# Kernel tuning notes

Measured on AMD Instinct MI355X. Metric: run time of the kernel, lower is better.

## Reference

```python
import jax, jax.numpy as jnp
import numpy as np

M, B, U, D = 65536, 128, 256, 512
USAGE_DECAY = 0.95

def _l2n(x, axis):
    # tf.nn.l2_normalize semantics (K.l2_normalize)
    return x / jnp.sqrt(jnp.maximum(jnp.sum(x * x, axis=axis, keepdims=True), 1e-12))

def _lstm_cell(x, h, c, kernel, rec_kernel, bias):
    # Keras LSTMCell: gates in order i, f, c, o
    z = x @ kernel + h @ rec_kernel + bias  # [B, 4U]
    zi, zf, zc, zo = jnp.split(z, 4, axis=-1)
    i = jax.nn.sigmoid(zi)
    f = jax.nn.sigmoid(zf)
    c_new = f * c + i * jnp.tanh(zc)
    o = jax.nn.sigmoid(zo)
    h_new = o * jnp.tanh(c_new)
    return h_new, c_new

def setup_inputs() -> dict:
    key = jax.random.key(0)
    ks = jax.random.split(key, 10)
    return {
        "inputs": jax.random.normal(ks[0], (B, D), jnp.float32),
        "r_tm1": jnp.zeros((B, U), jnp.float32),
        "m_tm1": jax.random.uniform(ks[1], (M, U), jnp.float32),
        "c_wu_tm1": jax.random.uniform(ks[2], (M, B), jnp.float32),
        "c_wlu_tm1": jnp.zeros((M, B), jnp.float32),
        "c_wr_tm1": jax.random.uniform(ks[3], (M, B), jnp.float32),
        "h_tm1": jax.random.normal(ks[4], (B, U), jnp.float32) * 0.1,
        "cc_tm1": jax.random.normal(ks[5], (B, U), jnp.float32) * 0.1,
        "kernel": jax.random.normal(ks[6], (D + U, 4 * U), jnp.float32) * 0.02,
        "rec_kernel": jax.random.normal(ks[7], (U, 4 * U), jnp.float32) * 0.02,
        "bias": jnp.zeros((4 * U,), jnp.float32),
        "write_gate": jax.random.normal(ks[8], (1,), jnp.float32),
    }

def reference(inputs, r_tm1, m_tm1, c_wu_tm1, c_wlu_tm1, c_wr_tm1,
              h_tm1, cc_tm1, kernel, rec_kernel, bias, write_gate):
    # Controller step on [inputs, r_tm1]
    ctrl_in = jnp.concatenate([inputs, r_tm1], axis=1)          # [B, D+U]
    key_list, cc = _lstm_cell(ctrl_in, h_tm1, cc_tm1, kernel, rec_kernel, bias)  # [B, U]

    wg = jax.nn.sigmoid(write_gate)                              # [1]
    # NOTE: faithful to source -- scalar (1 - wg) is ADDED elementwise, then c_wlu added
    c_ww = wg * c_wr_tm1 + (1.0 - wg) + c_wlu_tm1                # [M, B]

    # cosine-similarity addressing
    cos = _l2n(key_list, 1) @ _l2n(m_tm1, 1).T                   # [B, M]
    # K.softmax on the transposed matrix => softmax over the BATCH axis (faithful)
    c_wr = jax.nn.softmax(cos.T, axis=-1)                        # [M, B]
    read = c_wr.T @ m_tm1                                        # [B, U]

    c_wu = USAGE_DECAY * c_wu_tm1 + c_wr + c_ww                  # [M, B]

    # top_k(c_wu.T, M): v.T[-1,:] is the per-batch minimum over slots
    mins = jnp.min(c_wu, axis=0)                                 # [B]
    min_idx = jnp.argmin(c_wu, axis=0)                           # [B]
    b_star = jnp.argmin(mins)                                    # scalar
    i_star = min_idx[b_star]                                     # global least-used slot

    c_wlu = (c_wu <= mins[None, :]).astype(jnp.float32)          # [M, B]

    # zeroing_matrix = one_hot(i_star broadcast to B cols, on=0, off=1) [M,B];
    # dot(zeroing[M,B], ones[B,U]) -> rows = B except zeroed row (faithful B scaling)
    keep = 1.0 - jax.nn.one_hot(i_star, M, dtype=jnp.float32)    # [M]
    memory = (float(B) * keep)[:, None] * m_tm1                  # [M, U]
    memory = c_ww @ key_list + memory                            # [M, U]

    return (read, memory, c_wu, c_wlu, c_wr, key_list, cc)
```

## Files before the change

### kernel.cpp

```cpp
#include <hip/hip_runtime.h>
#include <math.h>

#define NM 65536
#define NB 128
#define NU 256
#define ND 512

constexpr size_t OUT_READ = 0;
constexpr size_t OUT_MEM  = 32768;
constexpr size_t OUT_CWU  = OUT_MEM + 16777216;
constexpr size_t OUT_CWLU = OUT_CWU + 8388608;
constexpr size_t OUT_CWR  = OUT_CWLU + 8388608;
constexpr size_t OUT_KEY  = OUT_CWR + 8388608;
constexpr size_t OUT_CC   = OUT_KEY + 32768;

constexpr size_t WS_KLNT   = 0;
constexpr size_t WS_MINENC = 131072;
constexpr size_t WS_MINS   = 132096;
constexpr size_t WS_ISTAR  = 132608;
constexpr size_t WS_PART   = 135168;

__device__ __forceinline__ unsigned fenc(float x) {
    unsigned u = __float_as_uint(x);
    return (u & 0x80000000u) ? ~u : (u | 0x80000000u);
}
__device__ __forceinline__ float fdec(unsigned e) {
    unsigned u = (e & 0x80000000u) ? (e ^ 0x80000000u) : ~e;
    return __uint_as_float(u);
}
__device__ __forceinline__ float sigm(float x) { return 1.0f / (1.0f + expf(-x)); }

__global__ __launch_bounds__(256) void k_lstm(
    const float* __restrict__ xin_g, const float* __restrict__ r_tm1,
    const float* __restrict__ h_tm1, const float* __restrict__ cc_tm1,
    const float* __restrict__ Wk, const float* __restrict__ Wr,
    const float* __restrict__ bias, float* __restrict__ out,
    float* __restrict__ klnT, unsigned long long* __restrict__ minenc)
{
    const int b = blockIdx.x, t = threadIdx.x;
    __shared__ float xin[ND + NU];
    __shared__ float hh[NU];
    __shared__ float red[NU];
    for (int k = t; k < ND; k += 256) xin[k] = xin_g[b * ND + k];
    xin[ND + t] = r_tm1[b * NU + t];
    hh[t] = h_tm1[b * NU + t];
    out[OUT_READ + b * NU + t] = 0.f;
    if (b == 0 && t < NB) minenc[t] = ~0ULL;
    __syncthreads();

    float zi = bias[t], zf = bias[NU + t], zc = bias[2 * NU + t], zo = bias[3 * NU + t];
    #pragma unroll 4
    for (int k = 0; k < ND + NU; ++k) {
        const float x = xin[k];
        const float* w = Wk + (size_t)k * (4 * NU);
        zi += x * w[t]; zf += x * w[NU + t]; zc += x * w[2 * NU + t]; zo += x * w[3 * NU + t];
    }
    #pragma unroll 4
    for (int k = 0; k < NU; ++k) {
        const float x = hh[k];
        const float* w = Wr + (size_t)k * (4 * NU);
        zi += x * w[t]; zf += x * w[NU + t]; zc += x * w[2 * NU + t]; zo += x * w[3 * NU + t];
    }
    const float gi = sigm(zi), gf = sigm(zf), gc = tanhf(zc), go = sigm(zo);
    const float cold = cc_tm1[b * NU + t];
    const float cn = __fadd_rn(__fmul_rn(gf, cold), __fmul_rn(gi, gc));
    const float hn = __fmul_rn(go, tanhf(cn));
    out[OUT_KEY + b * NU + t] = hn;
    out[OUT_CC + b * NU + t] = cn;
    red[t] = hn * hn;
    __syncthreads();
    for (int s = 128; s > 0; s >>= 1) { if (t < s) red[t] += red[t + s]; __syncthreads(); }
    const float nrm = sqrtf(fmaxf(red[0], 1e-12f));
    klnT[t * NB + b] = hn / nrm;
}

__global__ __launch_bounds__(256, 2) void k_dot(
    const float* __restrict__ mT, const float* __restrict__ klnT,
    const float* __restrict__ cwr_t, const float* __restrict__ cwlu_t,
    const float* __restrict__ cwu_t, const float* __restrict__ wgp,
    float* __restrict__ out, unsigned long long* __restrict__ minenc)
{
    __shared__ float smem[16384];
    __shared__ float rn_s[128];
    const int t = threadIdx.x, w = t >> 6, l = t & 63;
    const int tx = t & 15, ty = t >> 4;
    const int b0 = tx * 8, s0 = ty * 8;
    const int sb = blockIdx.x * 128;

    #pragma unroll 4
    for (int i = 0; i < 32; ++i) {
        const int s = w * 32 + i;
        const float4 mv = *(const float4*)(mT + (size_t)(sb + s) * NU + l * 4);
        float ss = mv.x * mv.x + mv.y * mv.y + mv.z * mv.z + mv.w * mv.w;
        #pragma unroll
        for (int d = 1; d < 64; d <<= 1) ss += __shfl_xor(ss, d);
        if (l == 0) rn_s[s] = sqrtf(fmaxf(ss, 1e-12f));
    }

    const int sl = t & 127, ug = t >> 7;
    const int ku_ = t >> 4, kb = (t & 15) * 4;

    float acc[8][8];
    #pragma unroll
    for (int i = 0; i < 8; ++i)
        #pragma unroll
        for (int j = 0; j < 8; ++j) acc[i][j] = 0.f;

    float4 gm[2], gk[2];
    #pragma unroll
    for (int i = 0; i < 2; ++i) {
        gm[i] = *(const float4*)(mT + (size_t)(sb + sl) * NU + (ug + 2 * i) * 4);
        gk[i] = *(const float4*)(klnT + (size_t)ku_ * NB + kb + i * 64);
    }
    for (int c = 0; c < 16; ++c) {
        const int mo = (c & 1) * 2048;
        const int ko = 4096 + (c & 1) * 2048;
        #pragma unroll
        for (int i = 0; i < 2; ++i) {
            const int uo = (ug + 2 * i) * 4;
            smem[mo + (uo + 0) * 128 + sl] = gm[i].x;
            smem[mo + (uo + 1) * 128 + sl] = gm[i].y;
            smem[mo + (uo + 2) * 128 + sl] = gm[i].z;
            smem[mo + (uo + 3) * 128 + sl] = gm[i].w;
            *(float4*)&smem[ko + ku_ * 128 + kb + i * 64] = gk[i];
        }
        __syncthreads();
        if (c < 15) {
            const int uc = (c + 1) * 16;
            #pragma unroll
            for (int i = 0; i < 2; ++i) {
                gm[i] = *(const float4*)(mT + (size_t)(sb + sl) * NU + uc + (ug + 2 * i) * 4);
                gk[i] = *(const float4*)(klnT + (size_t)(uc + ku_) * NB + kb + i * 64);
            }
        }
        #pragma unroll 4
        for (int u = 0; u < 16; ++u) {
            const float4 sv0 = *(const float4*)&smem[mo + u * 128 + s0];
            const float4 sv1 = *(const float4*)&smem[mo + u * 128 + s0 + 4];
            const float4 kv0 = *(const float4*)&smem[ko + u * 128 + b0];
            const float4 kv1 = *(const float4*)&smem[ko + u * 128 + b0 + 4];
            const float sv[8] = {sv0.x, sv0.y, sv0.z, sv0.w, sv1.x, sv1.y, sv1.z, sv1.w};
            const float kv[8] = {kv0.x, kv0.y, kv0.z, kv0.w, kv1.x, kv1.y, kv1.z, kv1.w};
            #pragma unroll
            for (int i = 0; i < 8; ++i)
                #pragma unroll
                for (int j = 0; j < 8; ++j)
                    acc[i][j] += sv[i] * kv[j];
        }
        __syncthreads();
    }

    #pragma unroll
    for (int i = 0; i < 8; ++i) {
        *(float4*)&smem[(s0 + i) * 128 + b0]     = make_float4(acc[i][0], acc[i][1], acc[i][2], acc[i][3]);
        *(float4*)&smem[(s0 + i) * 128 + b0 + 4] = make_float4(acc[i][4], acc[i][5], acc[i][6], acc[i][7]);
    }
    __syncthreads();

    const float wg = sigm(wgp[0]);
    const float omw = __fsub_rn(1.f, wg);
    unsigned long long lmin0 = ~0ULL, lmin1 = ~0ULL;
    #pragma unroll 2
    for (int i = 0; i < 32; ++i) {
        const int s = w * 32 + i;
        const int m = sb + s;
        const float2 dv = *(const float2*)&smem[s * 128 + 2 * l];
        const float rnv = rn_s[s];
        const float2 wrt = ((const float2*)(cwr_t + (size_t)m * NB))[l];
        const float2 wlu = ((const float2*)(cwlu_t + (size_t)m * NB))[l];
        const float2 wut = ((const float2*)(cwu_t + (size_t)m * NB))[l];
        const float c0 = dv.x / rnv, c1 = dv.y / rnv;
        float mx = fmaxf(c0, c1);
        #pragma unroll
        for (int d = 1; d < 64; d <<= 1) mx = fmaxf(mx, __shfl_xor(mx, d));
        const float e0 = expf(c0 - mx), e1 = expf(c1 - mx);
        float sm = e0 + e1;
        #pragma unroll
        for (int d = 1; d < 64; d <<= 1) sm += __shfl_xor(sm, d);
        const float w0 = e0 / sm, w1 = e1 / sm;
        const float cww0 = __fadd_rn(__fadd_rn(__fmul_rn(wg, wrt.x), omw), wlu.x);
        const float cww1 = __fadd_rn(__fadd_rn(__fmul_rn(wg, wrt.y), omw), wlu.y);
        const float cu0 = __fadd_rn(__fadd_rn(__fmul_rn(0.95f, wut.x), w0), cww0);
        const float cu1 = __fadd_rn(__fadd_rn(__fmul_rn(0.95f, wut.y), w1), cww1);
        ((float2*)(out + OUT_CWR))[(size_t)m * 64 + l] = make_float2(w0, w1);
        ((float2*)(out + OUT_CWU))[(size_t)m * 64 + l] = make_float2(cu0, cu1);
        const unsigned long long e0u = (((unsigned long long)fenc(cu0)) << 32) | (unsigned)m;
        const unsigned long long e1u = (((unsigned long long)fenc(cu1)) << 32) | (unsigned)m;
        lmin0 = (e0u < lmin0) ? e0u : lmin0;
        lmin1 = (e1u < lmin1) ? e1u : lmin1;
    }
    atomicMin(&minenc[2 * l], lmin0);
    atomicMin(&minenc[2 * l + 1], lmin1);
}

__global__ void k_argmin(const unsigned long long* __restrict__ minenc,
                         float* __restrict__ mins, unsigned* __restrict__ istar)
{
    __shared__ unsigned long long red[NB];
    const int t = threadIdx.x;
    const unsigned long long e = minenc[t];
    const unsigned enc32 = (unsigned)(e >> 32);
    mins[t] = fdec(enc32);
    red[t] = (((unsigned long long)enc32) << 32) | (unsigned)t;
    __syncthreads();
    for (int s = 64; s > 0; s >>= 1) {
        if (t < s) { const unsigned long long o = red[t + s]; if (o < red[t]) red[t] = o; }
        __syncthreads();
    }
    if (t == 0) {
        const unsigned bstar = (unsigned)(red[0] & 0xFFFFFFFFu);
        istar[0] = (unsigned)(minenc[bstar] & 0xFFFFFFFFu);
    }
}

__global__ __launch_bounds__(256, 1) void k_mem(
    const float* __restrict__ mT,
    const float* __restrict__ cwr_t, const float* __restrict__ cwlu_t,
    const float* __restrict__ wgp, const float* __restrict__ mins,
    const unsigned* __restrict__ istar_p, float* __restrict__ out)
{
    __shared__ float key[NB][NU];
    __shared__ float cww[32][NB];
    __shared__ float minsb[NB];
    const int t = threadIdx.x, w = t >> 6, l = t & 63;
    const int u0 = l * 4;
    const int sl = t >> 3, sb = (t & 7) * 16;

    for (int i = t; i < NB * NU / 4; i += 256)
        ((float4*)key)[i] = ((const float4*)(out + OUT_KEY))[i];
    if (t < NB) minsb[t] = mins[t];

    const float wg = sigm(wgp[0]);
    const float omw = __fsub_rn(1.f, wg);
    const int istar = (int)istar_p[0];
    const int base = blockIdx.x * 256;

    float4 wr[4], lu[4], wu[4], pm[8];
    #pragma unroll
    for (int k = 0; k < 4; ++k) {
        const size_t row = (size_t)(base + sl) * NB + sb + 4 * k;
        wr[k] = *(const float4*)(cwr_t + row);
        lu[k] = *(const float4*)(cwlu_t + row);
        wu[k] = *(const float4*)(out + OUT_CWU + row);
    }
    #pragma unroll
    for (int j = 0; j < 8; ++j)
        pm[j] = *(const float4*)(mT + (size_t)(base + w * 8 + j) * NU + u0);
    __syncthreads();

    for (int p = 0; p < 8; ++p) {
        const int sp = base + p * 32;
        #pragma unroll
        for (int k = 0; k < 4; ++k) {
            float4 cw;
            cw.x = __fadd_rn(__fadd_rn(__fmul_rn(wg, wr[k].x), omw), lu[k].x);
            cw.y = __fadd_rn(__fadd_rn(__fmul_rn(wg, wr[k].y), omw), lu[k].y);
            cw.z = __fadd_rn(__fadd_rn(__fmul_rn(wg, wr[k].z), omw), lu[k].z);
            cw.w = __fadd_rn(__fadd_rn(__fmul_rn(wg, wr[k].w), omw), lu[k].w);
            *(float4*)&cww[sl][sb + 4 * k] = cw;
            const float4 mb = *(const float4*)&minsb[sb + 4 * k];
            float4 wl;
            wl.x = (wu[k].x <= mb.x) ? 1.f : 0.f;
            wl.y = (wu[k].y <= mb.y) ? 1.f : 0.f;
            wl.z = (wu[k].z <= mb.z) ? 1.f : 0.f;
            wl.w = (wu[k].w <= mb.w) ? 1.f : 0.f;
            *(float4*)(out + OUT_CWLU + (size_t)(sp + sl) * NB + sb + 4 * k) = wl;
        }
        __syncthreads();
        float4 pmn[8];
        if (p < 7) {
            #pragma unroll
            for (int k = 0; k < 4; ++k) {
                const size_t row = (size_t)(sp + 32 + sl) * NB + sb + 4 * k;
                wr[k] = *(const float4*)(cwr_t + row);
                lu[k] = *(const float4*)(cwlu_t + row);
                wu[k] = *(const float4*)(out + OUT_CWU + row);
            }
            #pragma unroll
            for (int j = 0; j < 8; ++j)
                pmn[j] = *(const float4*)(mT + (size_t)(sp + 32 + w * 8 + j) * NU + u0);
        }
        float4 acc[8];
        #pragma unroll
        for (int j = 0; j < 8; ++j) acc[j] = make_float4(0.f, 0.f, 0.f, 0.f);
        for (int b0 = 0; b0 < NB; b0 += 4) {
            const float4 kv0 = *(const float4*)&key[b0 + 0][u0];
            const float4 kv1 = *(const float4*)&key[b0 + 1][u0];
            const float4 kv2 = *(const float4*)&key[b0 + 2][u0];
            const float4 kv3 = *(const float4*)&key[b0 + 3][u0];
            #pragma unroll
            for (int j = 0; j < 8; ++j) {
                const float4 cw = *(const float4*)&cww[w * 8 + j][b0];
                acc[j].x += cw.x * kv0.x; acc[j].y += cw.x * kv0.y; acc[j].z += cw.x * kv0.z; acc[j].w += cw.x * kv0.w;
                acc[j].x += cw.y * kv1.x; acc[j].y += cw.y * kv1.y; acc[j].z += cw.y * kv1.z; acc[j].w += cw.y * kv1.w;
                acc[j].x += cw.z * kv2.x; acc[j].y += cw.z * kv2.y; acc[j].z += cw.z * kv2.z; acc[j].w += cw.z * kv2.w;
                acc[j].x += cw.w * kv3.x; acc[j].y += cw.w * kv3.y; acc[j].z += cw.w * kv3.z; acc[j].w += cw.w * kv3.w;
            }
        }
        #pragma unroll
        for (int j = 0; j < 8; ++j) {
            const int s = sp + w * 8 + j;
            const float kf = (s == istar) ? 0.f : 128.f;
            float4 o;
            o.x = acc[j].x + kf * pm[j].x;
            o.y = acc[j].y + kf * pm[j].y;
            o.z = acc[j].z + kf * pm[j].z;
            o.w = acc[j].w + kf * pm[j].w;
            *(float4*)(out + OUT_MEM + (size_t)s * NU + u0) = o;
            if (p < 7) pm[j] = pmn[j];
        }
        __syncthreads();
    }
}

template <int USE_PART>
__global__ __launch_bounds__(256) void k_read(
    const float* __restrict__ mT, float* __restrict__ out, float* __restrict__ part)
{
    __shared__ float m_ch[2][8][128];
    __shared__ float cwr_ch[2][8][128];
    const int t = threadIdx.x;
    const int r = blockIdx.x, ri = r >> 1, uh = r & 1;
    const int s0 = ri * 256;
    const int b0 = (t & 15) * 8, u0 = (t >> 4) * 8;
    const int ssl = t >> 5, sul = (t & 31) * 4;

    float4 acc[8][2];
    #pragma unroll
    for (int bi = 0; bi < 8; ++bi) { acc[bi][0] = make_float4(0,0,0,0); acc[bi][1] = make_float4(0,0,0,0); }

    float4 pm = *(const float4*)(mT + (size_t)(s0 + ssl) * NU + uh * 128 + sul);
    float4 pc = *(const float4*)(out + OUT_CWR + (size_t)(s0 + ssl) * NB + sul);

    for (int c = 0; c < 32; ++c) {
        const int buf = c & 1;
        *(float4*)&m_ch[buf][ssl][sul] = pm;
        *(float4*)&cwr_ch[buf][ssl][sul] = pc;
        __syncthreads();
        if (c + 1 < 32) {
            const size_t sn = (size_t)(s0 + (c + 1) * 8 + ssl);
            pm = *(const float4*)(mT + sn * NU + uh * 128 + sul);
            pc = *(const float4*)(out + OUT_CWR + sn * NB + sul);
        }
        #pragma unroll
        for (int sj = 0; sj < 8; ++sj) {
            const float4 ca = *(const float4*)&cwr_ch[buf][sj][b0];
            const float4 cb = *(const float4*)&cwr_ch[buf][sj][b0 + 4];
            const float4 ma = *(const float4*)&m_ch[buf][sj][u0];
            const float4 mb = *(const float4*)&m_ch[buf][sj][u0 + 4];
            const float cwa[8] = {ca.x, ca.y, ca.z, ca.w, cb.x, cb.y, cb.z, cb.w};
            #pragma unroll
            for (int bi = 0; bi < 8; ++bi) {
                acc[bi][0].x += cwa[bi] * ma.x; acc[bi][0].y += cwa[bi] * ma.y;
                acc[bi][0].z += cwa[bi] * ma.z; acc[bi][0].w += cwa[bi] * ma.w;
                acc[bi][1].x += cwa[bi] * mb.x; acc[bi][1].y += cwa[bi] * mb.y;
                acc[bi][1].z += cwa[bi] * mb.z; acc[bi][1].w += cwa[bi] * mb.w;
            }
        }
    }

    if (USE_PART) {
        float* dst = part + (size_t)r * (128 * 128);
        #pragma unroll
        for (int bi = 0; bi < 8; ++bi) {
            *(float4*)(dst + (size_t)(b0 + bi) * 128 + u0) = acc[bi][0];
            *(float4*)(dst + (size_t)(b0 + bi) * 128 + u0 + 4) = acc[bi][1];
        }
    } else {
        #pragma unroll
        for (int bi = 0; bi < 8; ++bi) {
            const float v[8] = {acc[bi][0].x, acc[bi][0].y, acc[bi][0].z, acc[bi][0].w,
                                acc[bi][1].x, acc[bi][1].y, acc[bi][1].z, acc[bi][1].w};
            #pragma unroll
            for (int q = 0; q < 8; ++q)
                atomicAdd(out + OUT_READ + (size_t)(b0 + bi) * NU + uh * 128 + u0 + q, v[q]);
        }
    }
}

__global__ __launch_bounds__(256) void k_redread(const float* __restrict__ part,
                                                 float* __restrict__ out)
{
    const int b = blockIdx.x, u = threadIdx.x;
    const int uh = u >> 7, ul = u & 127;
    float s = 0.f;
    #pragma unroll 4
    for (int ri = 0; ri < 256; ++ri)
        s += part[((size_t)(ri * 2 + uh) * 128 + b) * 128 + ul];
    out[OUT_READ + b * NU + u] = s;
}

extern "C" void kernel_launch(void* const* d_in, const int* in_sizes, int n_in,
                              void* d_out, int out_size, void* d_ws, size_t ws_size,
                              hipStream_t stream)
{
    const float* inputs    = (const float*)d_in[0];
    const float* r_tm1     = (const float*)d_in[1];
    const float* m_tm1     = (const float*)d_in[2];
    const float* c_wu_tm1  = (const float*)d_in[3];
    const float* c_wlu_tm1 = (const float*)d_in[4];
    const float* c_wr_tm1  = (const float*)d_in[5];
    const float* h_tm1     = (const float*)d_in[6];
    const float* cc_tm1    = (const float*)d_in[7];
    const float* Wk        = (const float*)d_in[8];
    const float* Wr        = (const float*)d_in[9];
    const float* bias      = (const float*)d_in[10];
    const float* wgate     = (const float*)d_in[11];
    float* out = (float*)d_out;
    char* ws = (char*)d_ws;

    float* klnT = (float*)(ws + WS_KLNT);
    unsigned long long* minenc = (unsigned long long*)(ws + WS_MINENC);
    float* mins = (float*)(ws + WS_MINS);
    unsigned* istar = (unsigned*)(ws + WS_ISTAR);
    float* part = (float*)(ws + WS_PART);
    const bool use_part = ws_size >= WS_PART + (size_t)512 * 128 * 128 * 4;

    hipLaunchKernelGGL(k_lstm, dim3(128), dim3(256), 0, stream,
                       inputs, r_tm1, h_tm1, cc_tm1, Wk, Wr, bias, out, klnT, minenc);
    hipLaunchKernelGGL(k_dot, dim3(512), dim3(256), 0, stream,
                       m_tm1, klnT, c_wr_tm1, c_wlu_tm1, c_wu_tm1, wgate, out, minenc);
    hipLaunchKernelGGL(k_argmin, dim3(1), dim3(128), 0, stream, minenc, mins, istar);
    hipLaunchKernelGGL(k_mem, dim3(256), dim3(256), 0, stream,
                       m_tm1, c_wr_tm1, c_wlu_tm1, wgate, mins, istar, out);
    if (use_part) {
        hipLaunchKernelGGL((k_read<1>), dim3(512), dim3(256), 0, stream, m_tm1, out, part);
        hipLaunchKernelGGL(k_redread, dim3(128), dim3(256), 0, stream, part, out);
    } else {
        hipLaunchKernelGGL((k_read<0>), dim3(512), dim3(256), 0, stream, m_tm1, out, part);
    }
}
```

Baseline: 467.1 us.

## Shrink k_dot shared memory by streaming key tiles from registers and chunked epilogue

Restructures the cosine-similarity GEMM in k_dot. The key matrix is no longer staged in LDS; each thread keeps a small rotating register ring of key rows loaded straight from global/L2. Only 8-row memory slices are double-buffered in shared memory, and a single barrier per chunk replaces the previous two. The epilogue drains the accumulator tile in four 32-row chunks through a small padded buffer. Together these cut LDS from about 64KB to about 25KB, so more blocks can be resident per CU. The cost is more barriers in the epilogue, redundant global loads of the key matrix, and a changed thread-to-output mapping (strided rows and columns) that must stay consistent.

```diff
diff --git a/kernel.cpp b/kernel.cpp
--- a/kernel.cpp
+++ b/kernel.cpp
@@ -80,12 +80,13 @@
     const float* __restrict__ cwu_t, const float* __restrict__ wgp,
     float* __restrict__ out, unsigned long long* __restrict__ minenc)
 {
-    __shared__ float smem[16384];
+    __shared__ float ms[2][8][128];
+    __shared__ float sp[32][132];
     __shared__ float rn_s[128];
     const int t = threadIdx.x, w = t >> 6, l = t & 63;
     const int tx = t & 15, ty = t >> 4;
-    const int b0 = tx * 8, s0 = ty * 8;
     const int sb = blockIdx.x * 128;
+    const int sl = t & 127, ug = t >> 7;
 
     #pragma unroll 4
     for (int i = 0; i < 32; ++i) {
@@ -97,97 +98,95 @@
         if (l == 0) rn_s[s] = sqrtf(fmaxf(ss, 1e-12f));
     }
 
-    const int sl = t & 127, ug = t >> 7;
-    const int ku_ = t >> 4, kb = (t & 15) * 4;
-
     float acc[8][8];
     #pragma unroll
     for (int i = 0; i < 8; ++i)
         #pragma unroll
         for (int j = 0; j < 8; ++j) acc[i][j] = 0.f;
 
-    float4 gm[2], gk[2];
-    #pragma unroll
-    for (int i = 0; i < 2; ++i) {
-        gm[i] = *(const float4*)(mT + (size_t)(sb + sl) * NU + (ug + 2 * i) * 4);
-        gk[i] = *(const float4*)(klnT + (size_t)ku_ * NB + kb + i * 64);
-    }
-    for (int c = 0; c < 16; ++c) {
-        const int mo = (c & 1) * 2048;
-        const int ko = 4096 + (c & 1) * 2048;
-        #pragma unroll
-        for (int i = 0; i < 2; ++i) {
-            const int uo = (ug + 2 * i) * 4;
-            smem[mo + (uo + 0) * 128 + sl] = gm[i].x;
-            smem[mo + (uo + 1) * 128 + sl] = gm[i].y;
-            smem[mo + (uo + 2) * 128 + sl] = gm[i].z;
-            smem[mo + (uo + 3) * 128 + sl] = gm[i].w;
-            *(float4*)&smem[ko + ku_ * 128 + kb + i * 64] = gk[i];
-        }
-        __syncthreads();
-        if (c < 15) {
-            const int uc = (c + 1) * 16;
-            #pragma unroll
-            for (int i = 0; i < 2; ++i) {
-                gm[i] = *(const float4*)(mT + (size_t)(sb + sl) * NU + uc + (ug + 2 * i) * 4);
-                gk[i] = *(const float4*)(klnT + (size_t)(uc + ku_) * NB + kb + i * 64);
-            }
-        }
-        #pragma unroll 4
-        for (int u = 0; u < 16; ++u) {
-            const float4 sv0 = *(const float4*)&smem[mo + u * 128 + s0];
-            const float4 sv1 = *(const float4*)&smem[mo + u * 128 + s0 + 4];
-            const float4 kv0 = *(const float4*)&smem[ko + u * 128 + b0];
-            const float4 kv1 = *(const float4*)&smem[ko + u * 128 + b0 + 4];
-            const float sv[8] = {sv0.x, sv0.y, sv0.z, sv0.w, sv1.x, sv1.y, sv1.z, sv1.w};
-            const float kv[8] = {kv0.x, kv0.y, kv0.z, kv0.w, kv1.x, kv1.y, kv1.z, kv1.w};
+    float4 kva[4], kvb[4];
+    #pragma unroll
+    for (int u = 0; u < 4; ++u) {
+        kva[u] = *(const float4*)(klnT + (size_t)u * NB + tx * 4);
+        kvb[u] = *(const float4*)(klnT + (size_t)u * NB + tx * 4 + 64);
+    }
+    float4 gm = *(const float4*)(mT + (size_t)(sb + sl) * NU + ug * 4);
+
+    for (int c = 0; c < 32; ++c) {
+        const int cb = c & 1;
+        ms[cb][ug * 4 + 0][sl] = gm.x;
+        ms[cb][ug * 4 + 1][sl] = gm.y;
+        ms[cb][ug * 4 + 2][sl] = gm.z;
+        ms[cb][ug * 4 + 3][sl] = gm.w;
+        if (c < 31)
+            gm = *(const float4*)(mT + (size_t)(sb + sl) * NU + (c + 1) * 8 + ug * 4);
+        __syncthreads();
+        #pragma unroll
+        for (int u8 = 0; u8 < 8; ++u8) {
+            const int r = u8 & 3;
+            const float4 sv0 = *(const float4*)&ms[cb][u8][ty * 4];
+            const float4 sv1 = *(const float4*)&ms[cb][u8][64 + ty * 4];
+            const float svv[8] = {sv0.x, sv0.y, sv0.z, sv0.w, sv1.x, sv1.y, sv1.z, sv1.w};
+            const float kvv[8] = {kva[r].x, kva[r].y, kva[r].z, kva[r].w,
+                                  kvb[r].x, kvb[r].y, kvb[r].z, kvb[r].w};
             #pragma unroll
             for (int i = 0; i < 8; ++i)
                 #pragma unroll
                 for (int j = 0; j < 8; ++j)
-                    acc[i][j] += sv[i] * kv[j];
-        }
-        __syncthreads();
-    }
-
-    #pragma unroll
-    for (int i = 0; i < 8; ++i) {
-        *(float4*)&smem[(s0 + i) * 128 + b0]     = make_float4(acc[i][0], acc[i][1], acc[i][2], acc[i][3]);
-        *(float4*)&smem[(s0 + i) * 128 + b0 + 4] = make_float4(acc[i][4], acc[i][5], acc[i][6], acc[i][7]);
-    }
-    __syncthreads();
+                    acc[i][j] += svv[i] * kvv[j];
+            const int un = (c * 8 + u8 + 4) & 255;
+            kva[r] = *(const float4*)(klnT + (size_t)un * NB + tx * 4);
+            kvb[r] = *(const float4*)(klnT + (size_t)un * NB + tx * 4 + 64);
+        }
+    }
 
     const float wg = sigm(wgp[0]);
     const float omw = __fsub_rn(1.f, wg);
     unsigned long long lmin0 = ~0ULL, lmin1 = ~0ULL;
-    #pragma unroll 2
-    for (int i = 0; i < 32; ++i) {
-        const int s = w * 32 + i;
-        const int m = sb + s;
-        const float2 dv = *(const float2*)&smem[s * 128 + 2 * l];
-        const float rnv = rn_s[s];
-        const float2 wrt = ((const float2*)(cwr_t + (size_t)m * NB))[l];
-        const float2 wlu = ((const float2*)(cwlu_t + (size_t)m * NB))[l];
-        const float2 wut = ((const float2*)(cwu_t + (size_t)m * NB))[l];
-        const float c0 = dv.x / rnv, c1 = dv.y / rnv;
-        float mx = fmaxf(c0, c1);
-        #pragma unroll
-        for (int d = 1; d < 64; d <<= 1) mx = fmaxf(mx, __shfl_xor(mx, d));
-        const float e0 = expf(c0 - mx), e1 = expf(c1 - mx);
-        float sm = e0 + e1;
-        #pragma unroll
-        for (int d = 1; d < 64; d <<= 1) sm += __shfl_xor(sm, d);
-        const float w0 = e0 / sm, w1 = e1 / sm;
-        const float cww0 = __fadd_rn(__fadd_rn(__fmul_rn(wg, wrt.x), omw), wlu.x);
-        const float cww1 = __fadd_rn(__fadd_rn(__fmul_rn(wg, wrt.y), omw), wlu.y);
-        const float cu0 = __fadd_rn(__fadd_rn(__fmul_rn(0.95f, wut.x), w0), cww0);
-        const float cu1 = __fadd_rn(__fadd_rn(__fmul_rn(0.95f, wut.y), w1), cww1);
-        ((float2*)(out + OUT_CWR))[(size_t)m * 64 + l] = make_float2(w0, w1);
-        ((float2*)(out + OUT_CWU))[(size_t)m * 64 + l] = make_float2(cu0, cu1);
-        const unsigned long long e0u = (((unsigned long long)fenc(cu0)) << 32) | (unsigned)m;
-        const unsigned long long e1u = (((unsigned long long)fenc(cu1)) << 32) | (unsigned)m;
-        lmin0 = (e0u < lmin0) ? e0u : lmin0;
-        lmin1 = (e1u < lmin1) ? e1u : lmin1;
+    #pragma unroll
+    for (int g = 0; g < 4; ++g) {
+        if ((ty >> 3) == (g & 1)) {
+            const int h = g >> 1;
+            const int sl0 = (ty & 7) * 4;
+            #pragma unroll
+            for (int q = 0; q < 4; ++q) {
+                *(float4*)&sp[sl0 + q][tx * 4] =
+                    make_float4(acc[h * 4 + q][0], acc[h * 4 + q][1], acc[h * 4 + q][2], acc[h * 4 + q][3]);
+                *(float4*)&sp[sl0 + q][64 + tx * 4] =
+                    make_float4(acc[h * 4 + q][4], acc[h * 4 + q][5], acc[h * 4 + q][6], acc[h * 4 + q][7]);
+            }
+        }
+        __syncthreads();
+        #pragma unroll 2
+        for (int i = 0; i < 8; ++i) {
+            const int s = 32 * g + w * 8 + i;
+            const int m = sb + s;
+            const float2 dv = *(const float2*)&sp[s - 32 * g][2 * l];
+            const float rnv = rn_s[s];
+            const float2 wrt = ((const float2*)(cwr_t + (size_t)m * NB))[l];
+            const float2 wlu = ((const float2*)(cwlu_t + (size_t)m * NB))[l];
+            const float2 wut = ((const float2*)(cwu_t + (size_t)m * NB))[l];
+            const float c0 = dv.x / rnv, c1 = dv.y / rnv;
+            float mx = fmaxf(c0, c1);
+            #pragma unroll
+            for (int d = 1; d < 64; d <<= 1) mx = fmaxf(mx, __shfl_xor(mx, d));
+            const float e0 = expf(c0 - mx), e1 = expf(c1 - mx);
+            float sm = e0 + e1;
+            #pragma unroll
+            for (int d = 1; d < 64; d <<= 1) sm += __shfl_xor(sm, d);
+            const float w0 = e0 / sm, w1 = e1 / sm;
+            const float cww0 = __fadd_rn(__fadd_rn(__fmul_rn(wg, wrt.x), omw), wlu.x);
+            const float cww1 = __fadd_rn(__fadd_rn(__fmul_rn(wg, wrt.y), omw), wlu.y);
+            const float cu0 = __fadd_rn(__fadd_rn(__fmul_rn(0.95f, wut.x), w0), cww0);
+            const float cu1 = __fadd_rn(__fadd_rn(__fmul_rn(0.95f, wut.y), w1), cww1);
+            ((float2*)(out + OUT_CWR))[(size_t)m * 64 + l] = make_float2(w0, w1);
+            ((float2*)(out + OUT_CWU))[(size_t)m * 64 + l] = make_float2(cu0, cu1);
+            const unsigned long long e0u = (((unsigned long long)fenc(cu0)) << 32) | (unsigned)m;
+            const unsigned long long e1u = (((unsigned long long)fenc(cu1)) << 32) | (unsigned)m;
+            lmin0 = (e0u < lmin0) ? e0u : lmin0;
+            lmin1 = (e1u < lmin1) ? e1u : lmin1;
+        }
+        __syncthreads();
     }
     atomicMin(&minenc[2 * l], lmin0);
     atomicMin(&minenc[2 * l + 1], lmin1);
```

Result: no change. 472.6 us (+1.2%).

## Compute memory update GEMM with bf16 MFMA instead of fp32 FMA loops

Applied to the files above, without the earlier changes.

The k_mem kernel's c_ww @ key_list product is rewritten to use bf16 MFMA 16x16x32 instructions. c_ww and a transposed key tile are converted to bf16 in shared memory, and the grid is doubled to 512 blocks of 128 slots with two blocks per CU. This targets the scalar fp32 FMA cost of the M×B×U GEMM. It reduces precision of the memory output to bf16 inputs and drops the software prefetch of m_tm1, whose scalar non-vectorized loads and stores in the epilogue may cost bandwidth.

```diff
diff --git a/kernel.cpp b/kernel.cpp
--- a/kernel.cpp
+++ b/kernel.cpp
@@ -1,4 +1,5 @@
 #include <hip/hip_runtime.h>
+#include <hip/hip_bf16.h>
 #include <math.h>
 
 #define NM 65536
@@ -20,6 +21,9 @@
 constexpr size_t WS_ISTAR  = 132608;
 constexpr size_t WS_PART   = 135168;
 
+typedef __attribute__((ext_vector_type(8))) short short8v;
+typedef __attribute__((ext_vector_type(4))) float floatx4;
+
 __device__ __forceinline__ unsigned fenc(float x) {
     unsigned u = __float_as_uint(x);
     return (u & 0x80000000u) ? ~u : (u | 0x80000000u);
@@ -29,6 +33,10 @@
     return __uint_as_float(u);
 }
 __device__ __forceinline__ float sigm(float x) { return 1.0f / (1.0f + expf(-x)); }
+__device__ __forceinline__ unsigned short f2b(float f) {
+    __hip_bfloat16 h = __float2bfloat16(f);
+    return *reinterpret_cast<unsigned short*>(&h);
+}
 
 __global__ __launch_bounds__(256) void k_lstm(
     const float* __restrict__ xin_g, const float* __restrict__ r_tm1,
@@ -213,103 +221,99 @@
     }
 }
 
-__global__ __launch_bounds__(256, 1) void k_mem(
+__global__ __launch_bounds__(256, 2) void k_mem(
     const float* __restrict__ mT,
     const float* __restrict__ cwr_t, const float* __restrict__ cwlu_t,
     const float* __restrict__ wgp, const float* __restrict__ mins,
     const unsigned* __restrict__ istar_p, float* __restrict__ out)
 {
-    __shared__ float key[NB][NU];
-    __shared__ float cww[32][NB];
-    __shared__ float minsb[NB];
+    __shared__ unsigned short cwwb[128 * 136];
+    __shared__ unsigned short keyT[128 * 136];
     const int t = threadIdx.x, w = t >> 6, l = t & 63;
-    const int u0 = l * 4;
-    const int sl = t >> 3, sb = (t & 7) * 16;
-
-    for (int i = t; i < NB * NU / 4; i += 256)
-        ((float4*)key)[i] = ((const float4*)(out + OUT_KEY))[i];
-    if (t < NB) minsb[t] = mins[t];
-
+    const int sb = blockIdx.x * 128;
     const float wg = sigm(wgp[0]);
     const float omw = __fsub_rn(1.f, wg);
     const int istar = (int)istar_p[0];
-    const int base = blockIdx.x * 256;
-
-    float4 wr[4], lu[4], wu[4], pm[8];
-    #pragma unroll
-    for (int k = 0; k < 4; ++k) {
-        const size_t row = (size_t)(base + sl) * NB + sb + 4 * k;
-        wr[k] = *(const float4*)(cwr_t + row);
-        lu[k] = *(const float4*)(cwlu_t + row);
-        wu[k] = *(const float4*)(out + OUT_CWU + row);
-    }
-    #pragma unroll
-    for (int j = 0; j < 8; ++j)
-        pm[j] = *(const float4*)(mT + (size_t)(base + w * 8 + j) * NU + u0);
-    __syncthreads();
-
-    for (int p = 0; p < 8; ++p) {
-        const int sp = base + p * 32;
-        #pragma unroll
-        for (int k = 0; k < 4; ++k) {
+
+    {
+        const int srow = t >> 5;
+        const int bc = (t & 31) * 4;
+        for (int it = 0; it < 16; ++it) {
+            const int s = it * 8 + srow;
+            const size_t row = (size_t)(sb + s) * NB + bc;
+            const float4 wr = *(const float4*)(cwr_t + row);
+            const float4 lu = *(const float4*)(cwlu_t + row);
+            const float4 wu = *(const float4*)(out + OUT_CWU + row);
             float4 cw;
-            cw.x = __fadd_rn(__fadd_rn(__fmul_rn(wg, wr[k].x), omw), lu[k].x);
-            cw.y = __fadd_rn(__fadd_rn(__fmul_rn(wg, wr[k].y), omw), lu[k].y);
-            cw.z = __fadd_rn(__fadd_rn(__fmul_rn(wg, wr[k].z), omw), lu[k].z);
-            cw.w = __fadd_rn(__fadd_rn(__fmul_rn(wg, wr[k].w), omw), lu[k].w);
-            *(float4*)&cww[sl][sb + 4 * k] = cw;
-            const float4 mb = *(const float4*)&minsb[sb + 4 * k];
+            cw.x = __fadd_rn(__fadd_rn(__fmul_rn(wg, wr.x), omw), lu.x);
+            cw.y = __fadd_rn(__fadd_rn(__fmul_rn(wg, wr.y), omw), lu.y);
+            cw.z = __fadd_rn(__fadd_rn(__fmul_rn(wg, wr.z), omw), lu.z);
+            cw.w = __fadd_rn(__fadd_rn(__fmul_rn(wg, wr.w), omw), lu.w);
+            ushort4 pk;
+            pk.x = f2b(cw.x); pk.y = f2b(cw.y); pk.z = f2b(cw.z); pk.w = f2b(cw.w);
+            *(ushort4*)&cwwb[s * 136 + bc] = pk;
+            const float4 mb = *(const float4*)(mins + bc);
             float4 wl;
-            wl.x = (wu[k].x <= mb.x) ? 1.f : 0.f;
-            wl.y = (wu[k].y <= mb.y) ? 1.f : 0.f;
-            wl.z = (wu[k].z <= mb.z) ? 1.f : 0.f;
-            wl.w = (wu[k].w <= mb.w) ? 1.f : 0.f;
-            *(float4*)(out + OUT_CWLU + (size_t)(sp + sl) * NB + sb + 4 * k) = wl;
+            wl.x = (wu.x <= mb.x) ? 1.f : 0.f;
+            wl.y = (wu.y <= mb.y) ? 1.f : 0.f;
+            wl.z = (wu.z <= mb.z) ? 1.f : 0.f;
+            wl.w = (wu.w <= mb.w) ? 1.f : 0.f;
+            *(float4*)(out + OUT_CWLU + row) = wl;
+        }
+    }
+
+    const int rk = (l >> 4) * 8;
+    const int rr = l & 15;
+
+    for (int uh = 0; uh < 2; ++uh) {
+        if (uh) __syncthreads();
+        {
+            const int br = t >> 5;
+            const int ko = (t & 31) * 4;
+            for (int it = 0; it < 16; ++it) {
+                const int b = it * 8 + br;
+                const float4 kv = *(const float4*)(out + OUT_KEY + (size_t)b * NU + uh * 128 + ko);
+                keyT[(ko + 0) * 136 + b] = f2b(kv.x);
+                keyT[(ko + 1) * 136 + b] = f2b(kv.y);
+                keyT[(ko + 2) * 136 + b] = f2b(kv.z);
+                keyT[(ko + 3) * 136 + b] = f2b(kv.w);
+            }
         }
         __syncthreads();
-        float4 pmn[8];
-        if (p < 7) {
-            #pragma unroll
-            for (int k = 0; k < 4; ++k) {
-                const size_t row = (size_t)(sp + 32 + sl) * NB + sb + 4 * k;
-                wr[k] = *(const float4*)(cwr_t + row);
-                lu[k] = *(const float4*)(cwlu_t + row);
-                wu[k] = *(const float4*)(out + OUT_CWU + row);
+
+        floatx4 acc0[8], acc1[8];
+        #pragma unroll
+        for (int ut = 0; ut < 8; ++ut) {
+            acc0[ut] = (floatx4){0.f, 0.f, 0.f, 0.f};
+            acc1[ut] = (floatx4){0.f, 0.f, 0.f, 0.f};
+        }
+        #pragma unroll
+        for (int kc = 0; kc < 4; ++kc) {
+            const short8v a0 = *(const short8v*)&cwwb[(w * 32 + rr) * 136 + kc * 32 + rk];
+            const short8v a1 = *(const short8v*)&cwwb[(w * 32 + 16 + rr) * 136 + kc * 32 + rk];
+            #pragma unroll
+            for (int ut = 0; ut < 8; ++ut) {
+                const short8v bf = *(const short8v*)&keyT[(ut * 16 + rr) * 136 + kc * 32 + rk];
+                acc0[ut] = __builtin_amdgcn_mfma_f32_16x16x32_bf16(a0, bf, acc0[ut], 0, 0, 0);
+                acc1[ut] = __builtin_amdgcn_mfma_f32_16x16x32_bf16(a1, bf, acc1[ut], 0, 0, 0);
             }
-            #pragma unroll
-            for (int j = 0; j < 8; ++j)
-                pmn[j] = *(const float4*)(mT + (size_t)(sp + 32 + w * 8 + j) * NU + u0);
-        }
-        float4 acc[8];
-        #pragma unroll
-        for (int j = 0; j < 8; ++j) acc[j] = make_float4(0.f, 0.f, 0.f, 0.f);
-        for (int b0 = 0; b0 < NB; b0 += 4) {
-            const float4 kv0 = *(const float4*)&key[b0 + 0][u0];
-            const float4 kv1 = *(const float4*)&key[b0 + 1][u0];
-            const float4 kv2 = *(const float4*)&key[b0 + 2][u0];
-            const float4 kv3 = *(const float4*)&key[b0 + 3][u0];
-            #pragma unroll
-            for (int j = 0; j < 8; ++j) {
-                const float4 cw = *(const float4*)&cww[w * 8 + j][b0];
-                acc[j].x += cw.x * kv0.x; acc[j].y += cw.x * kv0.y; acc[j].z += cw.x * kv0.z; acc[j].w += cw.x * kv0.w;
-                acc[j].x += cw.y * kv1.x; acc[j].y += cw.y * kv1.y; acc[j].z += cw.y * kv1.z; acc[j].w += cw.y * kv1.w;
-                acc[j].x += cw.z * kv2.x; acc[j].y += cw.z * kv2.y; acc[j].z += cw.z * kv2.z; acc[j].w += cw.z * kv2.w;
-                acc[j].x += cw.w * kv3.x; acc[j].y += cw.w * kv3.y; acc[j].z += cw.w * kv3.z; acc[j].w += cw.w * kv3.w;
+        }
+
+        #pragma unroll
+        for (int ut = 0; ut < 8; ++ut) {
+            const int gcol = uh * 128 + ut * 16 + rr;
+            #pragma unroll
+            for (int q = 0; q < 4; ++q) {
+                const int grow0 = sb + w * 32 + (l >> 4) * 4 + q;
+                const int grow1 = grow0 + 16;
+                const float mv0 = mT[(size_t)grow0 * NU + gcol];
+                const float mv1 = mT[(size_t)grow1 * NU + gcol];
+                const float kf0 = (grow0 == istar) ? 0.f : 128.f;
+                const float kf1 = (grow1 == istar) ? 0.f : 128.f;
+                out[OUT_MEM + (size_t)grow0 * NU + gcol] = acc0[ut][q] + kf0 * mv0;
+                out[OUT_MEM + (size_t)grow1 * NU + gcol] = acc1[ut][q] + kf1 * mv1;
             }
         }
-        #pragma unroll
-        for (int j = 0; j < 8; ++j) {
-            const int s = sp + w * 8 + j;
-            const float kf = (s == istar) ? 0.f : 128.f;
-            float4 o;
-            o.x = acc[j].x + kf * pm[j].x;
-            o.y = acc[j].y + kf * pm[j].y;
-            o.z = acc[j].z + kf * pm[j].z;
-            o.w = acc[j].w + kf * pm[j].w;
-            *(float4*)(out + OUT_MEM + (size_t)s * NU + u0) = o;
-            if (p < 7) pm[j] = pmn[j];
-        }
-        __syncthreads();
     }
 }
 
@@ -421,7 +425,7 @@
     hipLaunchKernelGGL(k_dot, dim3(512), dim3(256), 0, stream,
                        m_tm1, klnT, c_wr_tm1, c_wlu_tm1, c_wu_tm1, wgate, out, minenc);
     hipLaunchKernelGGL(k_argmin, dim3(1), dim3(128), 0, stream, minenc, mins, istar);
-    hipLaunchKernelGGL(k_mem, dim3(256), dim3(256), 0, stream,
+    hipLaunchKernelGGL(k_mem, dim3(512), dim3(256), 0, stream,
                        m_tm1, c_wr_tm1, c_wlu_tm1, wgate, mins, istar, out);
     if (use_part) {
         hipLaunchKernelGGL((k_read<1>), dim3(512), dim3(256), 0, stream, m_tm1, out, part);
```

After: 423.5 us. 9.3% less time.
